# Optimization experiments

Hardware: AMD Instinct MI355X
Metric: run time of the kernel (lower is better)

## Reference

```python
import jax, jax.numpy as jnp
import numpy as np

H = 256  # hidden_size


def _gru_layer(x_seq, w_ih, w_hh, b_ih, b_hh, return_seq):
    """PyTorch-convention GRU layer.
    x_seq: [B, T, I]; w_ih: [3H, I]; w_hh: [3H, H]; biases: [3H].
    Gate order (torch): r, z, n.
    """
    B = x_seq.shape[0]
    # Precompute input-side gate projections for all timesteps (one big GEMM).
    gx = jnp.einsum('bti,gi->btg', x_seq, w_ih) + b_ih          # [B, T, 3H]
    gx = jnp.transpose(gx, (1, 0, 2))                            # [T, B, 3H]

    def step(h, gx_t):
        gh = h @ w_hh.T + b_hh                                   # [B, 3H]
        r = jax.nn.sigmoid(gx_t[:, :H] + gh[:, :H])
        z = jax.nn.sigmoid(gx_t[:, H:2 * H] + gh[:, H:2 * H])
        n = jnp.tanh(gx_t[:, 2 * H:] + r * gh[:, 2 * H:])
        h_new = (1.0 - z) * n + z * h
        return h_new, (h_new if return_seq else None)

    h0 = jnp.zeros((B, H), dtype=x_seq.dtype)
    h_last, ys = jax.lax.scan(step, h0, gx)
    if return_seq:
        return jnp.transpose(ys, (1, 0, 2))                      # [B, T, H]
    return h_last                                                # [B, H]


def setup_inputs() -> dict:
    key = jax.random.key(0)
    ks = jax.random.split(key, 11)
    s = 1.0 / np.sqrt(H)
    u = lambda k, shape: jax.random.uniform(k, shape, jnp.float32, -s, s)
    return {
        'x': jax.random.normal(ks[0], (512, 1024, 1), jnp.float32),
        'w_ih_l0': u(ks[1], (3 * H, 1)),
        'w_hh_l0': u(ks[2], (3 * H, H)),
        'b_ih_l0': u(ks[3], (3 * H,)),
        'b_hh_l0': u(ks[4], (3 * H,)),
        'w_ih_l1': u(ks[5], (3 * H, H)),
        'w_hh_l1': u(ks[6], (3 * H, H)),
        'b_ih_l1': u(ks[7], (3 * H,)),
        'b_hh_l1': u(ks[8], (3 * H,)),
        'w_fc': u(ks[9], (1, H)),
        'b_fc': u(ks[10], (1,)),
    }


def reference(x, w_ih_l0, w_hh_l0, b_ih_l0, b_hh_l0,
              w_ih_l1, w_hh_l1, b_ih_l1, b_hh_l1, w_fc, b_fc):
    # Inference mode: inter-layer dropout (p=0.2) is identity in eval.
    h0_seq = _gru_layer(x, w_ih_l0, w_hh_l0, b_ih_l0, b_hh_l0, return_seq=True)
    h_last = _gru_layer(h0_seq, w_ih_l1, w_hh_l1, b_ih_l1, b_hh_l1, return_seq=False)
    return h_last @ w_fc.T + b_fc                                # [B, 1]
```

## Files before the change

### kernel.cpp

```cpp
#include <hip/hip_runtime.h>


#define HH 256
#define TT 1024
#define BB 512
#define TC 64
#define NC (TT / TC)
#define NR (BB * TC)
#define F_GRID 320

typedef float    f32x4 __attribute__((ext_vector_type(4)));
typedef _Float16 f16x8 __attribute__((ext_vector_type(8)));

__device__ __forceinline__ int swz(int row, int col) {
    return row * 256 + ((((col >> 3) ^ (row & 7))) << 3) + (col & 7);
}
__device__ __forceinline__ float fsigm(float v) {
    return __builtin_amdgcn_rcpf(1.f + __expf(-v));
}
__device__ __forceinline__ float ftanh(float v) {
    return 1.f - 2.f * __builtin_amdgcn_rcpf(__expf(2.f * v) + 1.f);
}

template <int LAYER>
__device__ __forceinline__ void
rec_body(int rid, _Float16* sh, const _Float16* wfrag,
         const float* __restrict__ bhh, const float* __restrict__ bih,
         const float* __restrict__ x,
         const _Float16* __restrict__ gx3,
         const float* __restrict__ wih0,
         _Float16* __restrict__ h0c,
         float* __restrict__ hstate,
         int t0, bool first)
{
    const int tid = threadIdx.x;
    const int w = tid >> 6, l = tid & 63;
    const int cl = l & 15, kg = l >> 4;
    const int c0 = w * 32 + cl;
    const int r0 = kg * 4;
    const int b0 = rid * 16;

    f16x8 wf[6][8];
#pragma unroll
    for (int i6 = 0; i6 < 6; ++i6)
#pragma unroll
        for (int kk = 0; kk < 8; ++kk)
            wf[i6][kk] = *(const f16x8*)(wfrag + (size_t)(((w * 6 + i6) * 8 + kk) * 64 + l) * 8);

    float bias[2][4];
    float wi[2][3];
#pragma unroll
    for (int c2 = 0; c2 < 2; ++c2) {
        const int cc = c0 + c2 * 16;
        bias[c2][0] = bhh[cc] + bih[cc];
        bias[c2][1] = bhh[256 + cc] + bih[256 + cc];
        bias[c2][2] = bhh[512 + cc];
        bias[c2][3] = bih[512 + cc];
        if (LAYER == 0) {
            wi[c2][0] = wih0[cc]; wi[c2][1] = wih0[256 + cc]; wi[c2][2] = wih0[512 + cc];
        }
    }

    _Float16 hm[2][4];
#pragma unroll
    for (int c2 = 0; c2 < 2; ++c2)
#pragma unroll
        for (int j = 0; j < 4; ++j) {
            float v = first ? 0.f : hstate[(size_t)(b0 + r0 + j) * 256 + c0 + c2 * 16];
            hm[c2][j] = (_Float16)v;
            sh[swz(r0 + j, c0 + c2 * 16)] = hm[c2][j];
        }
    __syncthreads();

    for (int t = 0; t < TC; ++t) {
        const int cur = t & 1;

        float xv[4];
        _Float16 gv[3][2][4];
        if (LAYER == 0) {
#pragma unroll
            for (int j = 0; j < 4; ++j)
                xv[j] = x[(size_t)(b0 + r0 + j) * TT + t0 + t];
        } else {
#pragma unroll
            for (int g = 0; g < 3; ++g)
#pragma unroll
                for (int c2 = 0; c2 < 2; ++c2)
#pragma unroll
                    for (int j = 0; j < 4; ++j)
                        gv[g][c2][j] = gx3[((size_t)g * NR + (size_t)(b0 + r0 + j) * TC + t) * 256 + c0 + c2 * 16];
        }

        f32x4 acc[6];
#pragma unroll
        for (int i6 = 0; i6 < 6; ++i6) {
            acc[i6][0] = 0.f; acc[i6][1] = 0.f; acc[i6][2] = 0.f; acc[i6][3] = 0.f;
        }
        const _Float16* hb = sh + cur * 4096;
#pragma unroll
        for (int kk = 0; kk < 8; ++kk) {
            const int kb = kk * 4 + kg;
            f16x8 a = *(const f16x8*)(hb + cl * 256 + ((kb ^ (cl & 7)) << 3));
#pragma unroll
            for (int i6 = 0; i6 < 6; ++i6)
                acc[i6] = __builtin_amdgcn_mfma_f32_16x16x32_f16(a, wf[i6][kk], acc[i6], 0, 0, 0);
        }

        _Float16* hbn = sh + (cur ^ 1) * 4096;
#pragma unroll
        for (int c2 = 0; c2 < 2; ++c2) {
            const int cc = c0 + c2 * 16;
#pragma unroll
            for (int j = 0; j < 4; ++j) {
                float gr, gz, gn;
                if (LAYER == 0) {
                    gr = xv[j] * wi[c2][0]; gz = xv[j] * wi[c2][1]; gn = xv[j] * wi[c2][2];
                } else {
                    gr = (float)gv[0][c2][j]; gz = (float)gv[1][c2][j]; gn = (float)gv[2][c2][j];
                }
                const float r  = fsigm(acc[c2][j] + bias[c2][0] + gr);
                const float z  = fsigm(acc[2 + c2][j] + bias[c2][1] + gz);
                const float nn = ftanh(gn + bias[c2][3] + r * (acc[4 + c2][j] + bias[c2][2]));
                const float h  = nn + z * ((float)hm[c2][j] - nn);
                hm[c2][j] = (_Float16)h;
                hbn[swz(r0 + j, cc)] = hm[c2][j];
                if (LAYER == 0)
                    h0c[((size_t)(b0 + r0 + j) * TC + t) * 256 + cc] = hm[c2][j];
            }
        }
        __syncthreads();
    }

#pragma unroll
    for (int c2 = 0; c2 < 2; ++c2)
#pragma unroll
        for (int j = 0; j < 4; ++j)
            hstate[(size_t)(b0 + r0 + j) * 256 + c0 + c2 * 16] = (float)hm[c2][j];
}

__device__ __forceinline__ void
gemm_body(int gid, _Float16* Al, const _Float16* __restrict__ h0c,
          const _Float16* __restrict__ wi1h, _Float16* __restrict__ gx3)
{
    const int tid = threadIdx.x;
    const int m0 = gid * 128;
#pragma unroll
    for (int i = 0; i < 8; ++i) {
        const int u = i * 512 + tid;
        const int row = u >> 5, kb = u & 31;
        f32x4 d = *(const f32x4*)(const void*)(h0c + (size_t)(m0 + row) * 256 + kb * 8);
        *(f32x4*)&Al[row * 256 + ((kb ^ (row & 7)) << 3)] = d;
    }
    __syncthreads();

    const int w = tid >> 6, l = tid & 63;
    const int wm = w >> 2, wn = w & 3, cl = l & 15, kg = l >> 4;

    for (int g = 0; g < 3; ++g) {
        f32x4 acc[4][4];
#pragma unroll
        for (int mi = 0; mi < 4; ++mi)
#pragma unroll
            for (int ni = 0; ni < 4; ++ni) {
                acc[mi][ni][0] = 0.f; acc[mi][ni][1] = 0.f;
                acc[mi][ni][2] = 0.f; acc[mi][ni][3] = 0.f;
            }
#pragma unroll
        for (int kk = 0; kk < 8; ++kk) {
            const int kb = kk * 4 + kg;
            f16x8 av[4], bv[4];
#pragma unroll
            for (int mi = 0; mi < 4; ++mi) {
                const int row = wm * 64 + mi * 16 + cl;
                av[mi] = *(const f16x8*)&Al[row * 256 + ((kb ^ (row & 7)) << 3)];
            }
#pragma unroll
            for (int ni = 0; ni < 4; ++ni) {
                const int n = g * 256 + wn * 64 + ni * 16 + cl;
                bv[ni] = *(const f16x8*)(const void*)(wi1h + (size_t)n * 256 + kb * 8);
            }
#pragma unroll
            for (int mi = 0; mi < 4; ++mi)
#pragma unroll
                for (int ni = 0; ni < 4; ++ni)
                    acc[mi][ni] = __builtin_amdgcn_mfma_f32_16x16x32_f16(av[mi], bv[ni], acc[mi][ni], 0, 0, 0);
        }
#pragma unroll
        for (int mi = 0; mi < 4; ++mi)
#pragma unroll
            for (int ni = 0; ni < 4; ++ni)
#pragma unroll
                for (int j = 0; j < 4; ++j) {
                    const size_t m = m0 + wm * 64 + mi * 16 + kg * 4 + j;
                    const int n = wn * 64 + ni * 16 + cl;
                    gx3[((size_t)g * NR + m) * 256 + n] = (_Float16)acc[mi][ni][j];
                }
    }
}

__global__ void __launch_bounds__(512, 2)
F_kernel(int c,
         const _Float16* __restrict__ wfrag0, const _Float16* __restrict__ wfrag1,
         const _Float16* __restrict__ wi1h,
         const float* __restrict__ x, const float* __restrict__ wih0,
         const float* __restrict__ bih0, const float* __restrict__ bhh0,
         const float* __restrict__ bih1, const float* __restrict__ bhh1,
         _Float16* __restrict__ h0c_w, const _Float16* __restrict__ h0c_r,
         _Float16* __restrict__ gx_w, const _Float16* __restrict__ gx_r,
         float* __restrict__ h0st, float* __restrict__ h1st)
{
    __shared__ __align__(16) _Float16 smem[32768];
    const int bid = blockIdx.x;
    if (bid < 32) {
        if (c < NC)
            rec_body<0>(bid, smem, wfrag0, bhh0, bih0, x, nullptr, wih0,
                        h0c_w, h0st, c * TC, c == 0);
    } else if (bid < 64) {
        if (c >= 2)
            rec_body<1>(bid - 32, smem, wfrag1, bhh1, bih1, nullptr, gx_r, nullptr,
                        nullptr, h1st, 0, c == 2);
    } else {
        if (c >= 1 && c <= NC)
            gemm_body(bid - 64, smem, h0c_r, wi1h, gx_w);
    }
}

__global__ void __launch_bounds__(256)
prep_kernel(const float* __restrict__ whh0, const float* __restrict__ whh1,
            const float* __restrict__ wih1,
            _Float16* __restrict__ wfrag0, _Float16* __restrict__ wfrag1,
            _Float16* __restrict__ wi1h)
{
    const int u = blockIdx.x * 256 + threadIdx.x;
    const int sec = u / 24576;
    const int v = u % 24576;
    const float* src;
    _Float16* dst;
    int off;
    if (sec < 2) {
        const int l = v & 63, q = v >> 6;
        const int kk = q & 7, p = q >> 3;
        const int c2 = p & 1, t3 = p >> 1;
        const int g = t3 % 3, w = t3 / 3;
        off = (g * 256 + w * 32 + c2 * 16 + (l & 15)) * 256 + kk * 32 + (l >> 4) * 8;
        src = (sec == 0) ? whh0 : whh1;
        dst = (sec == 0) ? wfrag0 : wfrag1;
    } else {
        off = v * 8;
        src = wih1;
        dst = wi1h;
    }
    f32x4 f0 = *(const f32x4*)(src + off);
    f32x4 f1 = *(const f32x4*)(src + off + 4);
    f16x8 h;
    h[0] = (_Float16)f0[0]; h[1] = (_Float16)f0[1];
    h[2] = (_Float16)f0[2]; h[3] = (_Float16)f0[3];
    h[4] = (_Float16)f1[0]; h[5] = (_Float16)f1[1];
    h[6] = (_Float16)f1[2]; h[7] = (_Float16)f1[3];
    *(f16x8*)(dst + (size_t)v * 8) = h;
}

__global__ void __launch_bounds__(64)
fc_kernel(const float* __restrict__ h, const float* __restrict__ wfc,
          const float* __restrict__ bfc, float* __restrict__ out)
{
    const int b = blockIdx.x, l = threadIdx.x;
    f32x4 hv = *(const f32x4*)(h + (size_t)b * 256 + l * 4);
    f32x4 wv = *(const f32x4*)(wfc + l * 4);
    float s = hv[0] * wv[0] + hv[1] * wv[1] + hv[2] * wv[2] + hv[3] * wv[3];
#pragma unroll
    for (int off = 32; off; off >>= 1) s += __shfl_down(s, off);
    if (l == 0) out[b] = s + bfc[0];
}

extern "C" void kernel_launch(void* const* d_in, const int* in_sizes, int n_in,
                              void* d_out, int out_size, void* d_ws, size_t ws_size,
                              hipStream_t stream)
{
    (void)in_sizes; (void)n_in; (void)out_size;

    const float* x    = (const float*)d_in[0];
    const float* wih0 = (const float*)d_in[1];
    const float* whh0 = (const float*)d_in[2];
    const float* bih0 = (const float*)d_in[3];
    const float* bhh0 = (const float*)d_in[4];
    const float* wih1 = (const float*)d_in[5];
    const float* whh1 = (const float*)d_in[6];
    const float* bih1 = (const float*)d_in[7];
    const float* bhh1 = (const float*)d_in[8];
    const float* wfc  = (const float*)d_in[9];
    const float* bfc  = (const float*)d_in[10];
    float* out = (float*)d_out;

    char* p = (char*)d_ws;
    _Float16* wfrag0 = (_Float16*)p; p += (size_t)196608 * 2;
    _Float16* wfrag1 = (_Float16*)p; p += (size_t)196608 * 2;
    _Float16* wi1h   = (_Float16*)p; p += (size_t)196608 * 2;
    _Float16* h0c[2];
    h0c[0] = (_Float16*)p; p += (size_t)NR * 256 * 2;
    h0c[1] = (_Float16*)p; p += (size_t)NR * 256 * 2;
    _Float16* gxc[2];
    gxc[0] = (_Float16*)p; p += (size_t)3 * NR * 256 * 2;
    gxc[1] = (_Float16*)p; p += (size_t)3 * NR * 256 * 2;
    float* h0st = (float*)p; p += (size_t)BB * 256 * 4;
    float* h1st = (float*)p; p += (size_t)BB * 256 * 4;
    if ((size_t)(p - (char*)d_ws) > ws_size) return;

    prep_kernel<<<288, 256, 0, stream>>>(whh0, whh1, wih1, wfrag0, wfrag1, wi1h);

    for (int c = 0; c <= NC + 1; ++c) {
        F_kernel<<<F_GRID, 512, 0, stream>>>(
            c, wfrag0, wfrag1, wi1h, x, wih0,
            bih0, bhh0, bih1, bhh1,
            h0c[c & 1],
            h0c[(c ^ 1) & 1],
            gxc[(c ^ 1) & 1],
            gxc[c & 1],
            h0st, h1st);
    }
    fc_kernel<<<BB, 64, 0, stream>>>(h1st, wfc, bfc, out);
}
```

Before: 5.883 ms.

## Interleave recurrent output columns for paired f16x2 stores and stage x in LDS

Remaps the per-lane output columns so each lane owns two adjacent hidden columns (2*cl and 2*cl+1) instead of columns 16 apart. The weight-fragment prep is permuted to match, so LDS h writes, h0c/gx3 loads and stores, and hstate I/O become paired f16x2/f32x2 accesses. For layer 0 the x chunk is preloaded into padded LDS once per chunk, replacing a global load each timestep. Hidden state is also kept in fp32 registers between steps. Launch bounds drop to one block per SM minimum, which frees register budget but may reduce occupancy.

```diff
diff --git a/kernel.cpp b/kernel.cpp
--- a/kernel.cpp
+++ b/kernel.cpp
@@ -10,7 +10,9 @@
 #define F_GRID 320
 
 typedef float    f32x4 __attribute__((ext_vector_type(4)));
+typedef float    f32x2 __attribute__((ext_vector_type(2)));
 typedef _Float16 f16x8 __attribute__((ext_vector_type(8)));
+typedef _Float16 f16x2 __attribute__((ext_vector_type(2)));
 
 __device__ __forceinline__ int swz(int row, int col) {
     return row * 256 + ((((col >> 3) ^ (row & 7))) << 3) + (col & 7);
@@ -36,7 +38,7 @@
     const int tid = threadIdx.x;
     const int w = tid >> 6, l = tid & 63;
     const int cl = l & 15, kg = l >> 4;
-    const int c0 = w * 32 + cl;
+    const int cb = w * 32 + 2 * cl;
     const int r0 = kg * 4;
     const int b0 = rid * 16;
 
@@ -51,7 +53,7 @@
     float wi[2][3];
 #pragma unroll
     for (int c2 = 0; c2 < 2; ++c2) {
-        const int cc = c0 + c2 * 16;
+        const int cc = cb + c2;
         bias[c2][0] = bhh[cc] + bih[cc];
         bias[c2][1] = bhh[256 + cc] + bih[256 + cc];
         bias[c2][2] = bhh[512 + cc];
@@ -61,34 +63,40 @@
         }
     }
 
-    _Float16 hm[2][4];
-#pragma unroll
-    for (int c2 = 0; c2 < 2; ++c2)
-#pragma unroll
-        for (int j = 0; j < 4; ++j) {
-            float v = first ? 0.f : hstate[(size_t)(b0 + r0 + j) * 256 + c0 + c2 * 16];
-            hm[c2][j] = (_Float16)v;
-            sh[swz(r0 + j, c0 + c2 * 16)] = hm[c2][j];
-        }
+    float hm[2][4];
+#pragma unroll
+    for (int j = 0; j < 4; ++j) {
+        f32x2 v = {0.f, 0.f};
+        if (!first) v = *(const f32x2*)(hstate + (size_t)(b0 + r0 + j) * 256 + cb);
+        hm[0][j] = v[0]; hm[1][j] = v[1];
+        f16x2 hh; hh[0] = (_Float16)v[0]; hh[1] = (_Float16)v[1];
+        *(f16x2*)(sh + (r0 + j) * 256 + ((((cb >> 3) ^ ((r0 + j) & 7))) << 3) + (cb & 7)) = hh;
+    }
+
+    float* xsf = (float*)(sh + 8192);
+    if (LAYER == 0) {
+        const int row = tid >> 5, tc2 = (tid & 31) * 2;
+        const f32x2 d = *(const f32x2*)(x + (size_t)(b0 + row) * TT + t0 + tc2);
+        xsf[row * 65 + tc2] = d[0];
+        xsf[row * 65 + tc2 + 1] = d[1];
+    }
     __syncthreads();
 
     for (int t = 0; t < TC; ++t) {
         const int cur = t & 1;
 
         float xv[4];
-        _Float16 gv[3][2][4];
+        f16x2 gv[3][4];
         if (LAYER == 0) {
 #pragma unroll
             for (int j = 0; j < 4; ++j)
-                xv[j] = x[(size_t)(b0 + r0 + j) * TT + t0 + t];
+                xv[j] = xsf[(r0 + j) * 65 + t];
         } else {
 #pragma unroll
             for (int g = 0; g < 3; ++g)
 #pragma unroll
-                for (int c2 = 0; c2 < 2; ++c2)
-#pragma unroll
-                    for (int j = 0; j < 4; ++j)
-                        gv[g][c2][j] = gx3[((size_t)g * NR + (size_t)(b0 + r0 + j) * TC + t) * 256 + c0 + c2 * 16];
+                for (int j = 0; j < 4; ++j)
+                    gv[g][j] = *(const f16x2*)(gx3 + ((size_t)g * NR + (size_t)(b0 + r0 + j) * TC + t) * 256 + cb);
         }
 
         f32x4 acc[6];
@@ -108,34 +116,35 @@
 
         _Float16* hbn = sh + (cur ^ 1) * 4096;
 #pragma unroll
-        for (int c2 = 0; c2 < 2; ++c2) {
-            const int cc = c0 + c2 * 16;
-#pragma unroll
-            for (int j = 0; j < 4; ++j) {
+        for (int j = 0; j < 4; ++j) {
+            f16x2 hh;
+#pragma unroll
+            for (int c2 = 0; c2 < 2; ++c2) {
                 float gr, gz, gn;
                 if (LAYER == 0) {
                     gr = xv[j] * wi[c2][0]; gz = xv[j] * wi[c2][1]; gn = xv[j] * wi[c2][2];
                 } else {
-                    gr = (float)gv[0][c2][j]; gz = (float)gv[1][c2][j]; gn = (float)gv[2][c2][j];
+                    gr = (float)gv[0][j][c2]; gz = (float)gv[1][j][c2]; gn = (float)gv[2][j][c2];
                 }
                 const float r  = fsigm(acc[c2][j] + bias[c2][0] + gr);
                 const float z  = fsigm(acc[2 + c2][j] + bias[c2][1] + gz);
                 const float nn = ftanh(gn + bias[c2][3] + r * (acc[4 + c2][j] + bias[c2][2]));
-                const float h  = nn + z * ((float)hm[c2][j] - nn);
-                hm[c2][j] = (_Float16)h;
-                hbn[swz(r0 + j, cc)] = hm[c2][j];
-                if (LAYER == 0)
-                    h0c[((size_t)(b0 + r0 + j) * TC + t) * 256 + cc] = hm[c2][j];
+                const float h  = nn + z * (hm[c2][j] - nn);
+                hm[c2][j] = h;
+                hh[c2] = (_Float16)h;
             }
+            *(f16x2*)(hbn + (r0 + j) * 256 + ((((cb >> 3) ^ ((r0 + j) & 7))) << 3) + (cb & 7)) = hh;
+            if (LAYER == 0)
+                *(f16x2*)(h0c + ((size_t)(b0 + r0 + j) * TC + t) * 256 + cb) = hh;
         }
         __syncthreads();
     }
 
 #pragma unroll
-    for (int c2 = 0; c2 < 2; ++c2)
-#pragma unroll
-        for (int j = 0; j < 4; ++j)
-            hstate[(size_t)(b0 + r0 + j) * 256 + c0 + c2 * 16] = (float)hm[c2][j];
+    for (int j = 0; j < 4; ++j) {
+        f32x2 v; v[0] = hm[0][j]; v[1] = hm[1][j];
+        *(f32x2*)(hstate + (size_t)(b0 + r0 + j) * 256 + cb) = v;
+    }
 }
 
 __device__ __forceinline__ void
@@ -198,7 +207,7 @@
     }
 }
 
-__global__ void __launch_bounds__(512, 2)
+__global__ void __launch_bounds__(512, 1)
 F_kernel(int c,
          const _Float16* __restrict__ wfrag0, const _Float16* __restrict__ wfrag1,
          const _Float16* __restrict__ wi1h,
@@ -240,9 +249,10 @@
     if (sec < 2) {
         const int l = v & 63, q = v >> 6;
         const int kk = q & 7, p = q >> 3;
-        const int c2 = p & 1, t3 = p >> 1;
-        const int g = t3 % 3, w = t3 / 3;
-        off = (g * 256 + w * 32 + c2 * 16 + (l & 15)) * 256 + kk * 32 + (l >> 4) * 8;
+        const int i6 = p % 6, w = p / 6;
+        const int g = i6 >> 1, c2 = i6 & 1;
+        const int col = g * 256 + w * 32 + 2 * (l & 15) + c2;
+        off = col * 256 + kk * 32 + (l >> 4) * 8;
         src = (sec == 0) ? whh0 : whh1;
         dst = (sec == 0) ? wfrag0 : wfrag1;
     } else {
```

Measured after the change: 4.970 ms. 15.5% less time.

## Replace chunked multi-launch GRU with persistent wavefront kernel using global flag sync

Applied to the files above, without the earlier changes.

The per-chunk kernel launches, which needed staging of h0 chunks and a separate input-projection GEMM, are replaced by one persistent kernel of 192 blocks. Each batch group of 32 rows has 4 layer-0 blocks and 8 layer-1 blocks that split the hidden columns. The blocks exchange fp16 hidden states through global ring buffers and use acquire/release spin-wait flags, so layer 1 runs one step behind layer 0. Layer 1 now computes its input projection inline from layer-0 h, and all weights stay resident in LDS. This removes launch overhead and the large gx intermediate traffic, but every timestep now depends on cross-CU atomic spin synchronisation, and correctness relies on all 192 blocks being co-resident.

```diff
diff --git a/kernel.cpp b/kernel.cpp
--- a/kernel.cpp
+++ b/kernel.cpp
@@ -4,260 +4,329 @@
 #define HH 256
 #define TT 1024
 #define BB 512
-#define TC 64
-#define NC (TT / TC)
-#define NR (BB * TC)
-#define F_GRID 320
-
-typedef float    f32x4 __attribute__((ext_vector_type(4)));
-typedef _Float16 f16x8 __attribute__((ext_vector_type(8)));
-
-__device__ __forceinline__ int swz(int row, int col) {
-    return row * 256 + ((((col >> 3) ^ (row & 7))) << 3) + (col & 7);
-}
+#define NG 16
+
+typedef float        f32x4 __attribute__((ext_vector_type(4)));
+typedef int          i32x4 __attribute__((ext_vector_type(4)));
+typedef _Float16     f16x8 __attribute__((ext_vector_type(8)));
+typedef unsigned int uint;
+
 __device__ __forceinline__ float fsigm(float v) {
     return __builtin_amdgcn_rcpf(1.f + __expf(-v));
 }
 __device__ __forceinline__ float ftanh(float v) {
     return 1.f - 2.f * __builtin_amdgcn_rcpf(__expf(2.f * v) + 1.f);
 }
-
-template <int LAYER>
+__device__ __forceinline__ void spin_ge(uint* p, uint tgt) {
+    while (__hip_atomic_load(p, __ATOMIC_ACQUIRE, __HIP_MEMORY_SCOPE_AGENT) < tgt)
+        __builtin_amdgcn_s_sleep(1);
+}
+__device__ __forceinline__ uint ld_rel(const uint* p) {
+    return __hip_atomic_load(p, __ATOMIC_RELAXED, __HIP_MEMORY_SCOPE_AGENT);
+}
+__device__ __forceinline__ void st_rel(uint* p, uint v) {
+    __hip_atomic_store(p, v, __ATOMIC_RELAXED, __HIP_MEMORY_SCOPE_AGENT);
+}
+
+
 __device__ __forceinline__ void
-rec_body(int rid, _Float16* sh, const _Float16* wfrag,
-         const float* __restrict__ bhh, const float* __restrict__ bih,
-         const float* __restrict__ x,
-         const _Float16* __restrict__ gx3,
-         const float* __restrict__ wih0,
-         _Float16* __restrict__ h0c,
-         float* __restrict__ hstate,
-         int t0, bool first)
+rec0_body(int g, int m, _Float16* Wlds,
+          const _Float16* __restrict__ wl0, const float* __restrict__ x,
+          const float* __restrict__ bih0, const float* __restrict__ bhh0,
+          const float* __restrict__ wih0,
+          uint* hbuf0, uint* flags)
 {
     const int tid = threadIdx.x;
-    const int w = tid >> 6, l = tid & 63;
-    const int cl = l & 15, kg = l >> 4;
-    const int c0 = w * 32 + cl;
-    const int r0 = kg * 4;
-    const int b0 = rid * 16;
-
-    f16x8 wf[6][8];
-#pragma unroll
-    for (int i6 = 0; i6 < 6; ++i6)
-#pragma unroll
-        for (int kk = 0; kk < 8; ++kk)
-            wf[i6][kk] = *(const f16x8*)(wfrag + (size_t)(((w * 6 + i6) * 8 + kk) * 64 + l) * 8);
-
-    float bias[2][4];
-    float wi[2][3];
-#pragma unroll
-    for (int c2 = 0; c2 < 2; ++c2) {
-        const int cc = c0 + c2 * 16;
-        bias[c2][0] = bhh[cc] + bih[cc];
-        bias[c2][1] = bhh[256 + cc] + bih[256 + cc];
-        bias[c2][2] = bhh[512 + cc];
-        bias[c2][3] = bih[512 + cc];
-        if (LAYER == 0) {
-            wi[c2][0] = wih0[cc]; wi[c2][1] = wih0[256 + cc]; wi[c2][2] = wih0[512 + cc];
-        }
-    }
-
-    _Float16 hm[2][4];
-#pragma unroll
-    for (int c2 = 0; c2 < 2; ++c2)
-#pragma unroll
-        for (int j = 0; j < 4; ++j) {
-            float v = first ? 0.f : hstate[(size_t)(b0 + r0 + j) * 256 + c0 + c2 * 16];
-            hm[c2][j] = (_Float16)v;
-            sh[swz(r0 + j, c0 + c2 * 16)] = hm[c2][j];
-        }
+    const int w = tid >> 6, l = tid & 63, cl = l & 15, kg = l >> 4;
+
+    for (int i = 0; i < 24; ++i) {
+        int u = i * 256 + tid;
+        *(f32x4*)&Wlds[u * 8] = *(const f32x4*)(wl0 + ((size_t)m * 6144 + u) * 8);
+    }
+
+    const int c = m * 64 + w * 16 + cl;
+    const float b_r = bhh0[c] + bih0[c];
+    const float b_z = bhh0[HH + c] + bih0[HH + c];
+    const float b_nh = bhh0[2 * HH + c];
+    const float b_ni = bih0[2 * HH + c];
+    const float wir = wih0[c], wiz = wih0[HH + c], win = wih0[2 * HH + c];
+
+    float hm[8];
+#pragma unroll
+    for (int j = 0; j < 8; ++j) hm[j] = 0.f;
+
+    uint* f0 = flags + g * 16;
+    uint* c0 = flags + 256 + g * 16;
+    uint* hb_base = hbuf0 + (size_t)g * 4 * 4096;
     __syncthreads();
 
-    for (int t = 0; t < TC; ++t) {
-        const int cur = t & 1;
-
-        float xv[4];
-        _Float16 gv[3][2][4];
-        if (LAYER == 0) {
-#pragma unroll
-            for (int j = 0; j < 4; ++j)
-                xv[j] = x[(size_t)(b0 + r0 + j) * TT + t0 + t];
-        } else {
-#pragma unroll
-            for (int g = 0; g < 3; ++g)
-#pragma unroll
-                for (int c2 = 0; c2 < 2; ++c2)
-#pragma unroll
-                    for (int j = 0; j < 4; ++j)
-                        gv[g][c2][j] = gx3[((size_t)g * NR + (size_t)(b0 + r0 + j) * TC + t) * 256 + c0 + c2 * 16];
-        }
-
-        f32x4 acc[6];
-#pragma unroll
-        for (int i6 = 0; i6 < 6; ++i6) {
-            acc[i6][0] = 0.f; acc[i6][1] = 0.f; acc[i6][2] = 0.f; acc[i6][3] = 0.f;
-        }
-        const _Float16* hb = sh + cur * 4096;
-#pragma unroll
-        for (int kk = 0; kk < 8; ++kk) {
-            const int kb = kk * 4 + kg;
-            f16x8 a = *(const f16x8*)(hb + cl * 256 + ((kb ^ (cl & 7)) << 3));
-#pragma unroll
-            for (int i6 = 0; i6 < 6; ++i6)
-                acc[i6] = __builtin_amdgcn_mfma_f32_16x16x32_f16(a, wf[i6][kk], acc[i6], 0, 0, 0);
-        }
-
-        _Float16* hbn = sh + (cur ^ 1) * 4096;
-#pragma unroll
-        for (int c2 = 0; c2 < 2; ++c2) {
-            const int cc = c0 + c2 * 16;
+    for (int t = 0; t < TT; ++t) {
+        if (tid == 0) {
+            spin_ge(f0, 4u * t);
+            if (t >= 4) spin_ge(c0, 8u * (t - 3));
+        }
+        __syncthreads();
+
+        float xv[8];
+#pragma unroll
+        for (int j8 = 0; j8 < 8; ++j8) {
+            int row = (j8 >> 2) * 16 + kg * 4 + (j8 & 3);
+            xv[j8] = x[(size_t)(g * 32 + row) * TT + t];
+        }
+
+        uint* hbr = hb_base + ((t + 3) & 3) * 4096;
+        i32x4 av[2][8];
+#pragma unroll
+        for (int mt = 0; mt < 2; ++mt)
+#pragma unroll
+            for (int kk = 0; kk < 8; ++kk) {
+                int idx = (((kk * 4 + kg) * 32) + mt * 16 + cl) * 4;
+                i32x4 v;
+#pragma unroll
+                for (int d = 0; d < 4; ++d) v[d] = (int)ld_rel(hbr + idx + d);
+                av[mt][kk] = v;
+            }
+
+        f32x4 acc[2][3];
+#pragma unroll
+        for (int mt = 0; mt < 2; ++mt)
 #pragma unroll
             for (int j = 0; j < 4; ++j) {
-                float gr, gz, gn;
-                if (LAYER == 0) {
-                    gr = xv[j] * wi[c2][0]; gz = xv[j] * wi[c2][1]; gn = xv[j] * wi[c2][2];
-                } else {
-                    gr = (float)gv[0][c2][j]; gz = (float)gv[1][c2][j]; gn = (float)gv[2][c2][j];
+                acc[mt][0][j] = b_r; acc[mt][1][j] = b_z; acc[mt][2][j] = b_nh;
+            }
+#pragma unroll
+        for (int gi = 0; gi < 3; ++gi)
+#pragma unroll
+            for (int kk = 0; kk < 8; ++kk) {
+                f16x8 B = *(const f16x8*)&Wlds[(((((gi * 4 + w) * 8) + kk) * 4 + kg) * 16 + cl) * 8];
+#pragma unroll
+                for (int mt = 0; mt < 2; ++mt)
+                    acc[mt][gi] = __builtin_amdgcn_mfma_f32_16x16x32_f16(
+                        __builtin_bit_cast(f16x8, av[mt][kk]), B, acc[mt][gi], 0, 0, 0);
+            }
+
+        uint* hbw = hb_base + (t & 3) * 4096;
+#pragma unroll
+        for (int mt = 0; mt < 2; ++mt)
+#pragma unroll
+            for (int j = 0; j < 4; ++j) {
+                int j8 = mt * 4 + j;
+                int row = mt * 16 + kg * 4 + j;
+                float r  = fsigm(acc[mt][0][j] + xv[j8] * wir);
+                float z  = fsigm(acc[mt][1][j] + xv[j8] * wiz);
+                float nn = ftanh(xv[j8] * win + b_ni + r * acc[mt][2][j]);
+                float h  = nn + z * (hm[j8] - nn);
+                hm[j8] = h;
+                unsigned short hb16 = __builtin_bit_cast(unsigned short, (_Float16)h);
+                int other = __shfl_xor((int)hb16, 1);
+                if ((cl & 1) == 0) {
+                    uint word = (uint)hb16 | ((uint)(unsigned short)other << 16);
+                    st_rel(hbw + ((c >> 3) * 32 + row) * 4 + ((c & 7) >> 1), word);
                 }
-                const float r  = fsigm(acc[c2][j] + bias[c2][0] + gr);
-                const float z  = fsigm(acc[2 + c2][j] + bias[c2][1] + gz);
-                const float nn = ftanh(gn + bias[c2][3] + r * (acc[4 + c2][j] + bias[c2][2]));
-                const float h  = nn + z * ((float)hm[c2][j] - nn);
-                hm[c2][j] = (_Float16)h;
-                hbn[swz(r0 + j, cc)] = hm[c2][j];
-                if (LAYER == 0)
-                    h0c[((size_t)(b0 + r0 + j) * TC + t) * 256 + cc] = hm[c2][j];
-            }
-        }
+            }
         __syncthreads();
-    }
-
-#pragma unroll
-    for (int c2 = 0; c2 < 2; ++c2)
-#pragma unroll
-        for (int j = 0; j < 4; ++j)
-            hstate[(size_t)(b0 + r0 + j) * 256 + c0 + c2 * 16] = (float)hm[c2][j];
+        if (tid == 0)
+            __hip_atomic_fetch_add(f0, 1u, __ATOMIC_RELEASE, __HIP_MEMORY_SCOPE_AGENT);
+    }
 }
 
 __device__ __forceinline__ void
-gemm_body(int gid, _Float16* Al, const _Float16* __restrict__ h0c,
-          const _Float16* __restrict__ wi1h, _Float16* __restrict__ gx3)
+rec1_body(int g, int m, _Float16* Wlds,
+          const _Float16* __restrict__ wl1h, const _Float16* __restrict__ wl1i,
+          const float* __restrict__ bih1, const float* __restrict__ bhh1,
+          uint* hbuf0, uint* hbuf1, uint* flags, float* __restrict__ h1st)
 {
     const int tid = threadIdx.x;
-    const int m0 = gid * 128;
-#pragma unroll
-    for (int i = 0; i < 8; ++i) {
-        const int u = i * 512 + tid;
-        const int row = u >> 5, kb = u & 31;
-        f32x4 d = *(const f32x4*)(const void*)(h0c + (size_t)(m0 + row) * 256 + kb * 8);
-        *(f32x4*)&Al[row * 256 + ((kb ^ (row & 7)) << 3)] = d;
-    }
+    const int w = tid >> 6, l = tid & 63, cl = l & 15, kg = l >> 4;
+
+    for (int i = 0; i < 24; ++i) {
+        int u = i * 256 + tid;
+        const _Float16* src = (u < 3072)
+            ? (wl1h + ((size_t)m * 3072 + u) * 8)
+            : (wl1i + ((size_t)m * 3072 + (u - 3072)) * 8);
+        *(f32x4*)&Wlds[u * 8] = *(const f32x4*)src;
+    }
+
+    const bool act = (w < 2);
+    int c = 0;
+    float b_r = 0, b_z = 0, b_nh = 0, b_ni = 0;
+    if (act) {
+        c = m * 32 + w * 16 + cl;
+        b_r = bhh1[c] + bih1[c];
+        b_z = bhh1[HH + c] + bih1[HH + c];
+        b_nh = bhh1[2 * HH + c];
+        b_ni = bih1[2 * HH + c];
+    }
+    float hm[8];
+#pragma unroll
+    for (int j = 0; j < 8; ++j) hm[j] = 0.f;
+
+    uint* f0 = flags + g * 16;
+    uint* c0 = flags + 256 + g * 16;
+    uint* f1 = flags + 512 + g * 16;
+    uint* hb0 = hbuf0 + (size_t)g * 4 * 4096;
+    uint* hb1 = hbuf1 + (size_t)g * 2 * 4096;
     __syncthreads();
 
-    const int w = tid >> 6, l = tid & 63;
-    const int wm = w >> 2, wn = w & 3, cl = l & 15, kg = l >> 4;
-
-    for (int g = 0; g < 3; ++g) {
-        f32x4 acc[4][4];
-#pragma unroll
-        for (int mi = 0; mi < 4; ++mi)
-#pragma unroll
-            for (int ni = 0; ni < 4; ++ni) {
-                acc[mi][ni][0] = 0.f; acc[mi][ni][1] = 0.f;
-                acc[mi][ni][2] = 0.f; acc[mi][ni][3] = 0.f;
-            }
-#pragma unroll
-        for (int kk = 0; kk < 8; ++kk) {
-            const int kb = kk * 4 + kg;
-            f16x8 av[4], bv[4];
-#pragma unroll
-            for (int mi = 0; mi < 4; ++mi) {
-                const int row = wm * 64 + mi * 16 + cl;
-                av[mi] = *(const f16x8*)&Al[row * 256 + ((kb ^ (row & 7)) << 3)];
-            }
-#pragma unroll
-            for (int ni = 0; ni < 4; ++ni) {
-                const int n = g * 256 + wn * 64 + ni * 16 + cl;
-                bv[ni] = *(const f16x8*)(const void*)(wi1h + (size_t)n * 256 + kb * 8);
-            }
-#pragma unroll
-            for (int mi = 0; mi < 4; ++mi)
-#pragma unroll
-                for (int ni = 0; ni < 4; ++ni)
-                    acc[mi][ni] = __builtin_amdgcn_mfma_f32_16x16x32_f16(av[mi], bv[ni], acc[mi][ni], 0, 0, 0);
-        }
-#pragma unroll
-        for (int mi = 0; mi < 4; ++mi)
-#pragma unroll
-            for (int ni = 0; ni < 4; ++ni)
+    for (int t = 0; t < TT; ++t) {
+        if (tid == 0) {
+            spin_ge(f0, 4u * (t + 1));
+            spin_ge(f1, 8u * t);
+        }
+        __syncthreads();
+
+        if (act) {
+            f32x4 acc[2][4];
+#pragma unroll
+            for (int mt = 0; mt < 2; ++mt)
 #pragma unroll
                 for (int j = 0; j < 4; ++j) {
-                    const size_t m = m0 + wm * 64 + mi * 16 + kg * 4 + j;
-                    const int n = wn * 64 + ni * 16 + cl;
-                    gx3[((size_t)g * NR + m) * 256 + n] = (_Float16)acc[mi][ni][j];
+                    acc[mt][0][j] = b_r;  acc[mt][1][j] = b_z;
+                    acc[mt][2][j] = b_ni; acc[mt][3][j] = b_nh;
                 }
-    }
-}
-
-__global__ void __launch_bounds__(512, 2)
-F_kernel(int c,
-         const _Float16* __restrict__ wfrag0, const _Float16* __restrict__ wfrag1,
-         const _Float16* __restrict__ wi1h,
-         const float* __restrict__ x, const float* __restrict__ wih0,
-         const float* __restrict__ bih0, const float* __restrict__ bhh0,
-         const float* __restrict__ bih1, const float* __restrict__ bhh1,
-         _Float16* __restrict__ h0c_w, const _Float16* __restrict__ h0c_r,
-         _Float16* __restrict__ gx_w, const _Float16* __restrict__ gx_r,
-         float* __restrict__ h0st, float* __restrict__ h1st)
-{
-    __shared__ __align__(16) _Float16 smem[32768];
+
+            {
+                uint* hr = hb0 + (t & 3) * 4096;
+                i32x4 av[2][8];
+#pragma unroll
+                for (int mt = 0; mt < 2; ++mt)
+#pragma unroll
+                    for (int kk = 0; kk < 8; ++kk) {
+                        int idx = (((kk * 4 + kg) * 32) + mt * 16 + cl) * 4;
+                        i32x4 v;
+#pragma unroll
+                        for (int d = 0; d < 4; ++d) v[d] = (int)ld_rel(hr + idx + d);
+                        av[mt][kk] = v;
+                    }
+#pragma unroll
+                for (int gi = 0; gi < 3; ++gi)
+#pragma unroll
+                    for (int kk = 0; kk < 8; ++kk) {
+                        f16x8 B = *(const f16x8*)&Wlds[24576 + (((((gi * 2 + w) * 8) + kk) * 4 + kg) * 16 + cl) * 8];
+                        const int ai = (gi == 2) ? 2 : gi;
+#pragma unroll
+                        for (int mt = 0; mt < 2; ++mt)
+                            acc[mt][ai] = __builtin_amdgcn_mfma_f32_16x16x32_f16(
+                                __builtin_bit_cast(f16x8, av[mt][kk]), B, acc[mt][ai], 0, 0, 0);
+                    }
+            }
+            {
+                uint* hr = hb1 + ((t + 1) & 1) * 4096;
+                i32x4 av[2][8];
+#pragma unroll
+                for (int mt = 0; mt < 2; ++mt)
+#pragma unroll
+                    for (int kk = 0; kk < 8; ++kk) {
+                        int idx = (((kk * 4 + kg) * 32) + mt * 16 + cl) * 4;
+                        i32x4 v;
+#pragma unroll
+                        for (int d = 0; d < 4; ++d) v[d] = (int)ld_rel(hr + idx + d);
+                        av[mt][kk] = v;
+                    }
+#pragma unroll
+                for (int gi = 0; gi < 3; ++gi)
+#pragma unroll
+                    for (int kk = 0; kk < 8; ++kk) {
+                        f16x8 B = *(const f16x8*)&Wlds[(((((gi * 2 + w) * 8) + kk) * 4 + kg) * 16 + cl) * 8];
+                        const int ai = (gi == 2) ? 3 : gi;
+#pragma unroll
+                        for (int mt = 0; mt < 2; ++mt)
+                            acc[mt][ai] = __builtin_amdgcn_mfma_f32_16x16x32_f16(
+                                __builtin_bit_cast(f16x8, av[mt][kk]), B, acc[mt][ai], 0, 0, 0);
+                    }
+            }
+
+            uint* hbw = hb1 + (t & 1) * 4096;
+#pragma unroll
+            for (int mt = 0; mt < 2; ++mt)
+#pragma unroll
+                for (int j = 0; j < 4; ++j) {
+                    int j8 = mt * 4 + j;
+                    int row = mt * 16 + kg * 4 + j;
+                    float r  = fsigm(acc[mt][0][j]);
+                    float z  = fsigm(acc[mt][1][j]);
+                    float nn = ftanh(acc[mt][2][j] + r * acc[mt][3][j]);
+                    float h  = nn + z * (hm[j8] - nn);
+                    hm[j8] = h;
+                    unsigned short hb16 = __builtin_bit_cast(unsigned short, (_Float16)h);
+                    int other = __shfl_xor((int)hb16, 1);
+                    if ((cl & 1) == 0) {
+                        uint word = (uint)hb16 | ((uint)(unsigned short)other << 16);
+                        st_rel(hbw + ((c >> 3) * 32 + row) * 4 + ((c & 7) >> 1), word);
+                    }
+                    if (t == TT - 1)
+                        h1st[(size_t)(g * 32 + row) * HH + c] = h;
+                }
+        }
+        __syncthreads();
+        if (tid == 0) {
+            __hip_atomic_fetch_add(c0, 1u, __ATOMIC_RELAXED, __HIP_MEMORY_SCOPE_AGENT);
+            __hip_atomic_fetch_add(f1, 1u, __ATOMIC_RELEASE, __HIP_MEMORY_SCOPE_AGENT);
+        }
+    }
+}
+
+__global__ void __launch_bounds__(256)
+rec_all(const _Float16* __restrict__ wl0, const _Float16* __restrict__ wl1h,
+        const _Float16* __restrict__ wl1i,
+        const float* __restrict__ x, const float* __restrict__ wih0,
+        const float* __restrict__ bih0, const float* __restrict__ bhh0,
+        const float* __restrict__ bih1, const float* __restrict__ bhh1,
+        uint* hbuf0, uint* hbuf1, uint* flags, float* __restrict__ h1st)
+{
     const int bid = blockIdx.x;
-    if (bid < 32) {
-        if (c < NC)
-            rec_body<0>(bid, smem, wfrag0, bhh0, bih0, x, nullptr, wih0,
-                        h0c_w, h0st, c * TC, c == 0);
-    } else if (bid < 64) {
-        if (c >= 2)
-            rec_body<1>(bid - 32, smem, wfrag1, bhh1, bih1, nullptr, gx_r, nullptr,
-                        nullptr, h1st, 0, c == 2);
-    } else {
-        if (c >= 1 && c <= NC)
-            gemm_body(bid - 64, smem, h0c_r, wi1h, gx_w);
-    }
+    const int xcd = bid & 7, slot = bid >> 3;
+    const int g = xcd * 2 + (slot / 12);
+    const int s = slot % 12;
+    __shared__ __align__(16) _Float16 Wlds[49152];
+    if (s < 4)
+        rec0_body(g, s, Wlds, wl0, x, bih0, bhh0, wih0, hbuf0, flags);
+    else
+        rec1_body(g, s - 4, Wlds, wl1h, wl1i, bih1, bhh1, hbuf0, hbuf1, flags, h1st);
 }
 
 __global__ void __launch_bounds__(256)
 prep_kernel(const float* __restrict__ whh0, const float* __restrict__ whh1,
             const float* __restrict__ wih1,
-            _Float16* __restrict__ wfrag0, _Float16* __restrict__ wfrag1,
-            _Float16* __restrict__ wi1h)
+            _Float16* __restrict__ wl0, _Float16* __restrict__ wl1h,
+            _Float16* __restrict__ wl1i)
 {
     const int u = blockIdx.x * 256 + threadIdx.x;
-    const int sec = u / 24576;
-    const int v = u % 24576;
-    const float* src;
-    _Float16* dst;
-    int off;
-    if (sec < 2) {
-        const int l = v & 63, q = v >> 6;
-        const int kk = q & 7, p = q >> 3;
-        const int c2 = p & 1, t3 = p >> 1;
-        const int g = t3 % 3, w = t3 / 3;
-        off = (g * 256 + w * 32 + c2 * 16 + (l & 15)) * 256 + kk * 32 + (l >> 4) * 8;
-        src = (sec == 0) ? whh0 : whh1;
-        dst = (sec == 0) ? wfrag0 : wfrag1;
+    const float* src; _Float16* dst; int col, k0;
+    if (u < 24576) {
+        int m = u / 6144, r = u % 6144;
+        int cl = r & 15, kg = (r >> 4) & 3, kk = (r >> 6) & 7, nt = r >> 9;
+        col = (nt >> 2) * HH + m * 64 + (nt & 3) * 16 + cl;
+        k0 = (kk * 4 + kg) * 8;
+        src = whh0; dst = wl0 + (size_t)u * 8;
+    } else if (u < 49152) {
+        int v = u - 24576, m = v / 3072, r = v % 3072;
+        int cl = r & 15, kg = (r >> 4) & 3, kk = (r >> 6) & 7, nt = r >> 9;
+        col = (nt >> 1) * HH + m * 32 + (nt & 1) * 16 + cl;
+        k0 = (kk * 4 + kg) * 8;
+        src = whh1; dst = wl1h + (size_t)v * 8;
     } else {
-        off = v * 8;
-        src = wih1;
-        dst = wi1h;
-    }
-    f32x4 f0 = *(const f32x4*)(src + off);
-    f32x4 f1 = *(const f32x4*)(src + off + 4);
+        int v = u - 49152, m = v / 3072, r = v % 3072;
+        int cl = r & 15, kg = (r >> 4) & 3, kk = (r >> 6) & 7, nt = r >> 9;
+        col = (nt >> 1) * HH + m * 32 + (nt & 1) * 16 + cl;
+        k0 = (kk * 4 + kg) * 8;
+        src = wih1; dst = wl1i + (size_t)v * 8;
+    }
+    f32x4 f0 = *(const f32x4*)(src + (size_t)col * HH + k0);
+    f32x4 f1 = *(const f32x4*)(src + (size_t)col * HH + k0 + 4);
     f16x8 h;
     h[0] = (_Float16)f0[0]; h[1] = (_Float16)f0[1];
     h[2] = (_Float16)f0[2]; h[3] = (_Float16)f0[3];
     h[4] = (_Float16)f1[0]; h[5] = (_Float16)f1[1];
     h[6] = (_Float16)f1[2]; h[7] = (_Float16)f1[3];
-    *(f16x8*)(dst + (size_t)v * 8) = h;
+    *(f16x8*)dst = h;
+}
+
+__global__ void __launch_bounds__(256)
+init_kernel(uint* p, int n)
+{
+    int i = blockIdx.x * 256 + threadIdx.x;
+    if (i < n) p[i] = 0;
 }
 
 __global__ void __launch_bounds__(64)
@@ -265,7 +334,7 @@
           const float* __restrict__ bfc, float* __restrict__ out)
 {
     const int b = blockIdx.x, l = threadIdx.x;
-    f32x4 hv = *(const f32x4*)(h + (size_t)b * 256 + l * 4);
+    f32x4 hv = *(const f32x4*)(h + (size_t)b * HH + l * 4);
     f32x4 wv = *(const f32x4*)(wfc + l * 4);
     float s = hv[0] * wv[0] + hv[1] * wv[1] + hv[2] * wv[2] + hv[3] * wv[3];
 #pragma unroll
@@ -293,30 +362,20 @@
     float* out = (float*)d_out;
 
     char* p = (char*)d_ws;
-    _Float16* wfrag0 = (_Float16*)p; p += (size_t)196608 * 2;
-    _Float16* wfrag1 = (_Float16*)p; p += (size_t)196608 * 2;
-    _Float16* wi1h   = (_Float16*)p; p += (size_t)196608 * 2;
-    _Float16* h0c[2];
-    h0c[0] = (_Float16*)p; p += (size_t)NR * 256 * 2;
-    h0c[1] = (_Float16*)p; p += (size_t)NR * 256 * 2;
-    _Float16* gxc[2];
-    gxc[0] = (_Float16*)p; p += (size_t)3 * NR * 256 * 2;
-    gxc[1] = (_Float16*)p; p += (size_t)3 * NR * 256 * 2;
-    float* h0st = (float*)p; p += (size_t)BB * 256 * 4;
-    float* h1st = (float*)p; p += (size_t)BB * 256 * 4;
+    _Float16* wl0  = (_Float16*)p; p += (size_t)24576 * 8 * 2;
+    _Float16* wl1h = (_Float16*)p; p += (size_t)24576 * 8 * 2;
+    _Float16* wl1i = (_Float16*)p; p += (size_t)24576 * 8 * 2;
+    uint* hbuf0 = (uint*)p; p += (size_t)NG * 4 * 4096 * 4;
+    uint* hbuf1 = (uint*)p; p += (size_t)NG * 2 * 4096 * 4;
+    uint* flags = (uint*)p; p += 4096;
+    float* h1st = (float*)p; p += (size_t)BB * HH * 4;
     if ((size_t)(p - (char*)d_ws) > ws_size) return;
 
-    prep_kernel<<<288, 256, 0, stream>>>(whh0, whh1, wih1, wfrag0, wfrag1, wi1h);
-
-    for (int c = 0; c <= NC + 1; ++c) {
-        F_kernel<<<F_GRID, 512, 0, stream>>>(
-            c, wfrag0, wfrag1, wi1h, x, wih0,
-            bih0, bhh0, bih1, bhh1,
-            h0c[c & 1],
-            h0c[(c ^ 1) & 1],
-            gxc[(c ^ 1) & 1],
-            gxc[c & 1],
-            h0st, h1st);
-    }
+    const int nzero = NG * 4 * 4096 + NG * 2 * 4096 + 1024;
+    init_kernel<<<(nzero + 255) / 256, 256, 0, stream>>>(hbuf0, nzero);
+    prep_kernel<<<288, 256, 0, stream>>>(whh0, whh1, wih1, wl0, wl1h, wl1i);
+    rec_all<<<192, 256, 0, stream>>>(wl0, wl1h, wl1i, x, wih0,
+                                     bih0, bhh0, bih1, bhh1,
+                                     hbuf0, hbuf1, flags, h1st);
     fc_kernel<<<BB, 64, 0, stream>>>(h1st, wfc, bfc, out);
 }
```

Measured after the change: 10.81 ms. 1.84x slower.
